# Kernel optimization log

Hardware: AMD Instinct MI355X
Metric: run time of the kernel (lower is better)

The kernel has to match this reference:

```python
import jax, jax.numpy as jnp
import numpy as np

MARGIN = 0.7
SINKHORN_ITERS = 500


def setup_inputs() -> dict:
    key = jax.random.key(0)
    k1, k2, k3, k4, k5 = jax.random.split(key, 5)
    D, m, n = 2048, 2048, 2048
    query_features = jax.random.normal(k1, (D, m), dtype=jnp.float32)
    target_features = jax.random.normal(k2, (D, n), dtype=jnp.float32)
    # positive marginals (mu.log() / nu.log() must be finite), normalized to sum 1
    qa = jax.random.uniform(k3, (m,), dtype=jnp.float32, minval=0.1, maxval=1.0)
    ta = jax.random.uniform(k4, (n,), dtype=jnp.float32, minval=0.1, maxval=1.0)
    query_attention = qa / qa.sum()
    target_attention = ta / ta.sum()
    # contrastive label: 1 = positive pair, 0 = negative
    label = (jax.random.uniform(k5, (m,)) < 0.5).astype(jnp.float32)
    return {
        "query_features": query_features,
        "query_attention": query_attention,
        "target_features": target_features,
        "target_attention": target_attention,
        "label": label,
    }


def _pairwise_sq_dist(x, y):
    # x: [m, D], y: [n, D] -> squared euclidean distances [m, n], clamped at 0
    x2 = jnp.sum(x * x, axis=1)[:, None]
    y2 = jnp.sum(y * y, axis=1)[None, :]
    d = x2 + y2 - 2.0 * (x @ y.T)
    return jnp.maximum(d, 0.0)


def _log_sinkhorn(Z, log_mu, log_nu, iters):
    # Z: [m, n]; log-space Sinkhorn, matching torch version with batch dim squeezed
    u0 = jnp.zeros_like(log_mu)
    v0 = jnp.zeros_like(log_nu)

    def body(_, uv):
        u, v = uv
        u = log_mu - jax.nn.logsumexp(Z + v[None, :], axis=1)
        v = log_nu - jax.nn.logsumexp(Z + u[:, None], axis=0)
        return (u, v)

    u, v = jax.lax.fori_loop(0, iters, body, (u0, v0))
    return Z + u[:, None] + v[None, :]


def reference(query_features, query_attention, target_features, target_attention, label):
    qf = query_features.T  # [m, D]
    tf = target_features.T  # [n, D]
    M = _pairwise_sq_dist(qf, tf)  # [m, n]
    logP = _log_sinkhorn(M, jnp.log(query_attention), jnp.log(target_attention), SINKHORN_ITERS)
    P = jnp.exp(logP)  # [m, n]
    # per-query-descriptor residual between weighted query and OT-transported target
    resid = query_attention[:, None] * qf - P @ tf  # [m, D]
    distance = jnp.linalg.norm(resid, axis=1)  # [m]
    loss = 0.5 * label * distance ** 2 + 0.5 * (1.0 - label) * jnp.maximum(MARGIN - distance, 0.0) ** 2
    return loss.sum()
```

## Files before the change

kernel.cpp:

```cpp
#include <hip/hip_runtime.h>
#include <math.h>

#define S 2048
#define MARGIN 0.7f
#define ITERS 500
#define NBLK 256
#define TPB 512
#define NREP 8

typedef unsigned long long u64;

#define SLOT_STRIDE 16384

__global__ __launch_bounds__(256) void init_marg_k(const float* __restrict__ qa,
                                                   const float* __restrict__ ta,
                                                   float* __restrict__ lmu,
                                                   float* __restrict__ lnu,
                                                   float* __restrict__ vt,
                                                   float* __restrict__ dist2,
                                                   u64* __restrict__ valU,
                                                   u64* __restrict__ valV) {
  int i = blockIdx.x * 256 + threadIdx.x;
  lmu[i] = __logf(qa[i]);
  lnu[i] = __logf(ta[i]);
  vt[i] = 0.f;
  dist2[i] = 0.f;
  const u64 poison = 0xFFFFFFFF00000000ull;
#pragma unroll
  for (int k = 0; k < 16; ++k) {
    valU[i + (k << 11)] = poison;
    valV[i + (k << 11)] = poison;
  }
}

__global__ __launch_bounds__(256) void colsumsq_k(const float* __restrict__ TF,
                                                  float* __restrict__ vt) {
  int jb = blockIdx.x & 7, dc = blockIdx.x >> 3;
  int j = jb * 256 + threadIdx.x;
  int d0 = dc * 256;
  float acc = 0.f;
  for (int d = d0; d < d0 + 256; ++d) {
    float v = TF[d * S + j];
    acc = fmaf(v, v, acc);
  }
  atomicAdd(&vt[j], acc);
}

__global__ __launch_bounds__(256) void pack_v0_k(const float* __restrict__ vt,
                                                 u64* __restrict__ valV) {
  int i = blockIdx.x * 256 + threadIdx.x;
  u64 w = (1ull << 32) | (u64)__float_as_uint(vt[i]);
#pragma unroll
  for (int r = 0; r < NREP; ++r) valV[(r << 11) + i] = w;
}

__global__ __launch_bounds__(256) void gemm_tn_k(const float* __restrict__ A,
                                                 const float* __restrict__ B,
                                                 float* __restrict__ C, float alpha) {
  __shared__ float As[16][128];
  __shared__ float Bs[16][128];
  int t = threadIdx.x;
  int i0 = blockIdx.y * 128, j0 = blockIdx.x * 128;
  int tx = t & 15, ty = t >> 4;
  float acc[8][8];
#pragma unroll
  for (int r = 0; r < 8; ++r)
#pragma unroll
    for (int c = 0; c < 8; ++c) acc[r][c] = 0.f;

  int e = t * 4;
  int dd0 = e >> 7, ii = e & 127;
  int dd1 = dd0 + 8;
  for (int k0 = 0; k0 < S; k0 += 16) {
    float4 a0 = *(const float4*)&A[(k0 + dd0) * S + i0 + ii];
    float4 b0 = *(const float4*)&B[(k0 + dd0) * S + j0 + ii];
    float4 a1 = *(const float4*)&A[(k0 + dd1) * S + i0 + ii];
    float4 b1 = *(const float4*)&B[(k0 + dd1) * S + j0 + ii];
    __syncthreads();
    *(float4*)&As[dd0][ii] = a0; *(float4*)&Bs[dd0][ii] = b0;
    *(float4*)&As[dd1][ii] = a1; *(float4*)&Bs[dd1][ii] = b1;
    __syncthreads();
#pragma unroll
    for (int kk = 0; kk < 16; ++kk) {
      float a[8], b[8];
      *(float4*)&a[0] = *(const float4*)&As[kk][ty * 8];
      *(float4*)&a[4] = *(const float4*)&As[kk][ty * 8 + 4];
      *(float4*)&b[0] = *(const float4*)&Bs[kk][tx * 4];
      *(float4*)&b[4] = *(const float4*)&Bs[kk][64 + tx * 4];
#pragma unroll
      for (int r = 0; r < 8; ++r)
#pragma unroll
        for (int c = 0; c < 8; ++c) acc[r][c] = fmaf(a[r], b[c], acc[r][c]);
    }
  }
#pragma unroll
  for (int r = 0; r < 8; ++r) {
    int i = i0 + ty * 8 + r;
    float4 o0 = make_float4(acc[r][0] * alpha, acc[r][1] * alpha, acc[r][2] * alpha, acc[r][3] * alpha);
    float4 o1 = make_float4(acc[r][4] * alpha, acc[r][5] * alpha, acc[r][6] * alpha, acc[r][7] * alpha);
    *(float4*)&C[i * S + j0 + tx * 4] = o0;
    *(float4*)&C[i * S + j0 + 64 + tx * 4] = o1;
  }
}

__global__ __launch_bounds__(256) void transpose_k(const float* __restrict__ in,
                                                   float* __restrict__ out) {
  __shared__ float tile[64][65];
  int i0 = blockIdx.y * 64, j0 = blockIdx.x * 64;
  int tx = threadIdx.x & 63, ty = threadIdx.x >> 6;
#pragma unroll
  for (int r = 0; r < 16; ++r) {
    int row = r * 4 + ty;
    tile[row][tx] = in[(i0 + row) * S + j0 + tx];
  }
  __syncthreads();
#pragma unroll
  for (int r = 0; r < 16; ++r) {
    int row = r * 4 + ty;
    out[(j0 + row) * S + i0 + tx] = tile[tx][row];
  }
}

#define PADD(P, A) P.x += A.x; P.y += A.y; P.z += A.z; P.w += A.w
#define PMAX(P) fmaxf(fmaxf(P.x, P.y), fmaxf(P.z, P.w))
#define PEXPS(P) (__expf(P.x - m) + __expf(P.y - m) + __expf(P.z - m) + __expf(P.w - m))
#define ALD(p) __hip_atomic_load((p), __ATOMIC_RELAXED, __HIP_MEMORY_SCOPE_AGENT)

__device__ __forceinline__ unsigned consume(const u64* __restrict__ base,
                                            unsigned ph,
                                            float* __restrict__ s_pot,
                                            unsigned* __restrict__ s_chgW,
                                            int t, int wv, int lane) {
  if (t < 64) {
    unsigned got = 0;
    const int L0 = t << 2;
    while (got != 0xFu) {
#pragma unroll
      for (int k = 0; k < 4; ++k)
        if (!(got & (1u << k)))
          if ((unsigned)(ALD(&base[(L0 + k) << 3]) >> 33) == ph)
            got |= 1u << k;
    }
  }
  __syncthreads();
  const int e = t << 2;
  u64 w0 = ALD(&base[e + 0]);
  u64 w1 = ALD(&base[e + 1]);
  u64 w2 = ALD(&base[e + 2]);
  u64 w3 = ALD(&base[e + 3]);
  unsigned ok = 0;
  do {
    if (!(ok & 1u)) { if ((unsigned)(w0 >> 33) == ph) ok |= 1u; else w0 = ALD(&base[e + 0]); }
    if (!(ok & 2u)) { if ((unsigned)(w1 >> 33) == ph) ok |= 2u; else w1 = ALD(&base[e + 1]); }
    if (!(ok & 4u)) { if ((unsigned)(w2 >> 33) == ph) ok |= 4u; else w2 = ALD(&base[e + 2]); }
    if (!(ok & 8u)) { if ((unsigned)(w3 >> 33) == ph) ok |= 8u; else w3 = ALD(&base[e + 3]); }
  } while (ok != 0xFu);
  unsigned chg = (unsigned)((w0 | w1 | w2 | w3) >> 32) & 1u;
  *(float4*)&s_pot[e] = make_float4(__uint_as_float((unsigned)w0),
                                    __uint_as_float((unsigned)w1),
                                    __uint_as_float((unsigned)w2),
                                    __uint_as_float((unsigned)w3));
  unsigned long long any = __ballot(chg != 0u);
  if (lane == 0) s_chgW[wv] = (any != 0ull) ? 1u : 0u;
  __syncthreads();
  return s_chgW[0] | s_chgW[1] | s_chgW[2] | s_chgW[3] |
         s_chgW[4] | s_chgW[5] | s_chgW[6] | s_chgW[7];
}

__device__ __forceinline__ float lse_row(const float* __restrict__ grow,
                                         const float* __restrict__ s_pot,
                                         int lane) {
  int j0 = lane << 2;
  float4 p0 = *(const float4*)&s_pot[j0];
  float4 p1 = *(const float4*)&s_pot[j0 + 256];
  float4 p2 = *(const float4*)&s_pot[j0 + 512];
  float4 p3 = *(const float4*)&s_pot[j0 + 768];
  float4 p4 = *(const float4*)&s_pot[j0 + 1024];
  float4 p5 = *(const float4*)&s_pot[j0 + 1280];
  float4 p6 = *(const float4*)&s_pot[j0 + 1536];
  float4 p7 = *(const float4*)&s_pot[j0 + 1792];
  float4 a0 = *(const float4*)&grow[j0];
  float4 a1 = *(const float4*)&grow[j0 + 256];
  float4 a2 = *(const float4*)&grow[j0 + 512];
  float4 a3 = *(const float4*)&grow[j0 + 768];
  float4 a4 = *(const float4*)&grow[j0 + 1024];
  float4 a5 = *(const float4*)&grow[j0 + 1280];
  float4 a6 = *(const float4*)&grow[j0 + 1536];
  float4 a7 = *(const float4*)&grow[j0 + 1792];
  PADD(p0, a0); PADD(p1, a1); PADD(p2, a2); PADD(p3, a3);
  PADD(p4, a4); PADD(p5, a5); PADD(p6, a6); PADD(p7, a7);
  float m0 = PMAX(p0), m1 = PMAX(p1), m2 = PMAX(p2), m3 = PMAX(p3);
  float m4 = PMAX(p4), m5 = PMAX(p5), m6 = PMAX(p6), m7 = PMAX(p7);
  m0 = fmaxf(m0, m1); m2 = fmaxf(m2, m3); m4 = fmaxf(m4, m5); m6 = fmaxf(m6, m7);
  float m = fmaxf(fmaxf(m0, m2), fmaxf(m4, m6));
#pragma unroll
  for (int off = 32; off; off >>= 1) m = fmaxf(m, __shfl_xor(m, off));
  float s = PEXPS(p0) + PEXPS(p1) + PEXPS(p2) + PEXPS(p3) +
            PEXPS(p4) + PEXPS(p5) + PEXPS(p6) + PEXPS(p7);
#pragma unroll
  for (int off = 32; off; off >>= 1) s += __shfl_xor(s, off);
  return m + __logf(s);
}

__global__ __launch_bounds__(TPB) void sinkhorn_k(
    const float* __restrict__ Gp, const float* __restrict__ GpT,
    const float* __restrict__ lmu, const float* __restrict__ lnu,
    float* __restrict__ ut, float* __restrict__ vt,
    u64* __restrict__ valU, u64* __restrict__ valV) {
  __shared__ float s_gu[8 * S];
  __shared__ float s_gv[8 * S];
  __shared__ float s_pot[S];
  __shared__ float s_res[8];
  __shared__ unsigned s_resC[8];
  __shared__ unsigned s_chgW[8];

  const int t = threadIdx.x;
  const int wv = t >> 6, lane = t & 63;
  const int bid = (int)blockIdx.x;
  const int row = (bid << 3) + wv;
  const int rep = bid & (NREP - 1);

  {
    const float* gu = Gp + (size_t)row * S;
    const float* gv = GpT + (size_t)row * S;
    float* lgu = s_gu + wv * S;
    float* lgv = s_gv + wv * S;
#pragma unroll
    for (int c = 0; c < 8; ++c) {
      int j = (lane << 2) + (c << 8);
      *(float4*)&lgu[j] = *(const float4*)&gu[j];
      *(float4*)&lgv[j] = *(const float4*)&gv[j];
    }
  }
  const float lmu_r = lmu[row];
  const float lnu_r = lnu[row];
  const float* grow_u = s_gu + wv * S;
  const float* grow_v = s_gv + wv * S;
  float prevU = __uint_as_float(0x7fc00000u);
  float prevV = prevU;
  float uLast = 0.f, vLast = 0.f;
  __syncthreads();

  for (int it = 0; it < ITERS; ++it) {
    const size_t so = (size_t)(it & 1) * SLOT_STRIDE;
    const unsigned phv = 2u * (unsigned)it;

    unsigned changed = consume(valV + so + ((size_t)rep << 11), phv,
                               s_pot, s_chgW, t, wv, lane);
    if (changed == 0u) break;
    {
      float nu = lmu_r - lse_row(grow_u, s_pot, lane);
      uLast = nu;
      if (lane == 0) {
        s_res[wv] = nu;
        s_resC[wv] = (__float_as_uint(nu) != __float_as_uint(prevU)) ? 1u : 0u;
        prevU = nu;
      }
    }
    __syncthreads();
    if (t < 64) {
      int jj = t & 7;
      u64 w = ((u64)(((phv + 1u) << 1) | s_resC[jj]) << 32) |
              (u64)__float_as_uint(s_res[jj]);
      __hip_atomic_store(&valU[so + ((size_t)(t >> 3) << 11) + (bid << 3) + jj],
                         w, __ATOMIC_RELAXED, __HIP_MEMORY_SCOPE_AGENT);
    }

    changed = consume(valU + so + ((size_t)rep << 11), phv + 1u,
                      s_pot, s_chgW, t, wv, lane);
    if (changed == 0u) break;
    {
      float nv = lnu_r - lse_row(grow_v, s_pot, lane);
      vLast = nv;
      if (lane == 0) {
        s_res[wv] = nv;
        s_resC[wv] = (__float_as_uint(nv) != __float_as_uint(prevV)) ? 1u : 0u;
        prevV = nv;
      }
    }
    __syncthreads();
    {
      const size_t so2 = (size_t)((it + 1) & 1) * SLOT_STRIDE;
      if (t < 64) {
        int jj = t & 7;
        u64 w = ((u64)(((phv + 2u) << 1) | s_resC[jj]) << 32) |
                (u64)__float_as_uint(s_res[jj]);
        __hip_atomic_store(&valV[so2 + ((size_t)(t >> 3) << 11) + (bid << 3) + jj],
                           w, __ATOMIC_RELAXED, __HIP_MEMORY_SCOPE_AGENT);
      }
    }
  }
  if (lane == 0) {
    ut[row] = uLast;
    vt[row] = vLast;
  }
}

__global__ __launch_bounds__(256) void rt_gemm_k(const float* __restrict__ TF,
                                                 const float* __restrict__ GpT,
                                                 const float* __restrict__ ut,
                                                 const float* __restrict__ vt,
                                                 float* __restrict__ RT) {
  __shared__ float As[16][128];
  __shared__ float Bs[16][128];
  int t = threadIdx.x;
  int d0 = blockIdx.y * 128, i0 = blockIdx.x * 128;
  int tx = t & 15, ty = t >> 4;
  float acc[8][8];
#pragma unroll
  for (int r = 0; r < 8; ++r)
#pragma unroll
    for (int c = 0; c < 8; ++c) acc[r][c] = 0.f;

  int akk = (t * 4) & 15, add0 = t >> 2;
  int eb = t * 4;
  int bkk0 = eb >> 7, bii = eb & 127, bkk1 = bkk0 + 8;
  float4 u4 = *(const float4*)&ut[i0 + bii];

  for (int k0 = 0; k0 < S; k0 += 16) {
    float4 av0 = *(const float4*)&TF[(d0 + add0) * S + k0 + akk];
    float4 av1 = *(const float4*)&TF[(d0 + add0 + 64) * S + k0 + akk];
    float4 g0 = *(const float4*)&GpT[(k0 + bkk0) * S + i0 + bii];
    float4 g1 = *(const float4*)&GpT[(k0 + bkk1) * S + i0 + bii];
    float v0 = vt[k0 + bkk0], v1 = vt[k0 + bkk1];
    __syncthreads();
    As[akk + 0][add0] = av0.x; As[akk + 1][add0] = av0.y;
    As[akk + 2][add0] = av0.z; As[akk + 3][add0] = av0.w;
    As[akk + 0][add0 + 64] = av1.x; As[akk + 1][add0 + 64] = av1.y;
    As[akk + 2][add0 + 64] = av1.z; As[akk + 3][add0 + 64] = av1.w;
    float4 p0 = make_float4(__expf(g0.x + u4.x + v0), __expf(g0.y + u4.y + v0),
                            __expf(g0.z + u4.z + v0), __expf(g0.w + u4.w + v0));
    float4 p1 = make_float4(__expf(g1.x + u4.x + v1), __expf(g1.y + u4.y + v1),
                            __expf(g1.z + u4.z + v1), __expf(g1.w + u4.w + v1));
    *(float4*)&Bs[bkk0][bii] = p0;
    *(float4*)&Bs[bkk1][bii] = p1;
    __syncthreads();
#pragma unroll
    for (int kk = 0; kk < 16; ++kk) {
      float a[8], b[8];
      *(float4*)&a[0] = *(const float4*)&As[kk][ty * 8];
      *(float4*)&a[4] = *(const float4*)&As[kk][ty * 8 + 4];
      *(float4*)&b[0] = *(const float4*)&Bs[kk][tx * 4];
      *(float4*)&b[4] = *(const float4*)&Bs[kk][64 + tx * 4];
#pragma unroll
      for (int r = 0; r < 8; ++r)
#pragma unroll
        for (int c = 0; c < 8; ++c) acc[r][c] = fmaf(a[r], b[c], acc[r][c]);
    }
  }
#pragma unroll
  for (int r = 0; r < 8; ++r) {
    int d = d0 + ty * 8 + r;
    *(float4*)&RT[d * S + i0 + tx * 4] = *(float4*)&acc[r][0];
    *(float4*)&RT[d * S + i0 + 64 + tx * 4] = *(float4*)&acc[r][4];
  }
}

__global__ __launch_bounds__(256) void dist2_partial_k(const float* __restrict__ QF,
                                                       const float* __restrict__ RT,
                                                       const float* __restrict__ qa,
                                                       float* __restrict__ dist2) {
  int ib = blockIdx.x & 7, dc = blockIdx.x >> 3;
  int i = ib * 256 + threadIdx.x;
  float qai = qa[i];
  float acc = 0.f;
  int d0 = dc * 256;
  for (int d = d0; d < d0 + 256; ++d) {
    float q = QF[d * S + i];
    float r = RT[d * S + i];
    float x = fmaf(qai, q, -r);
    acc = fmaf(x, x, acc);
  }
  atomicAdd(&dist2[i], acc);
}

__global__ __launch_bounds__(256) void loss_final_k(const float* __restrict__ dist2,
                                                    const float* __restrict__ label,
                                                    float* __restrict__ out) {
  int t = threadIdx.x;
  float acc = 0.f;
#pragma unroll
  for (int k = 0; k < 8; ++k) {
    int i = t + k * 256;
    float d2 = dist2[i];
    float dist = sqrtf(d2);
    float lab = label[i];
    float neg = fmaxf(MARGIN - dist, 0.f);
    acc += 0.5f * lab * d2 + 0.5f * (1.f - lab) * neg * neg;
  }
#pragma unroll
  for (int off = 32; off; off >>= 1) acc += __shfl_xor(acc, off);
  __shared__ float wsum[4];
  int wave = t >> 6, lane = t & 63;
  if (lane == 0) wsum[wave] = acc;
  __syncthreads();
  if (t == 0) out[0] = wsum[0] + wsum[1] + wsum[2] + wsum[3];
}

extern "C" void kernel_launch(void* const* d_in, const int* in_sizes, int n_in,
                              void* d_out, int out_size, void* d_ws, size_t ws_size,
                              hipStream_t stream) {
  const float* QF  = (const float*)d_in[0];
  const float* qa  = (const float*)d_in[1];
  const float* TF  = (const float*)d_in[2];
  const float* ta  = (const float*)d_in[3];
  const float* lab = (const float*)d_in[4];
  float* out = (float*)d_out;

  float* ws = (float*)d_ws;
  float* Gp    = ws;
  float* GpT   = Gp + S * S;
  float* ut    = GpT + S * S;
  float* vt    = ut + S;
  float* lmu   = vt + S;
  float* lnu   = lmu + S;
  float* dist2 = lnu + S;
  u64* valU = (u64*)(dist2 + S);
  u64* valV = valU + 2 * SLOT_STRIDE;

  init_marg_k<<<8, 256, 0, stream>>>(qa, ta, lmu, lnu, vt, dist2, valU, valV);
  colsumsq_k<<<64, 256, 0, stream>>>(TF, vt);
  pack_v0_k<<<8, 256, 0, stream>>>(vt, valV);
  gemm_tn_k<<<dim3(16, 16), 256, 0, stream>>>(QF, TF, Gp, -2.0f);
  transpose_k<<<dim3(32, 32), 256, 0, stream>>>(Gp, GpT);

  {
    const float* cGp = Gp; const float* cGpT = GpT;
    const float* clmu = lmu; const float* clnu = lnu;
    float* cut = ut; float* cvt = vt;
    u64* cvalU = valU; u64* cvalV = valV;
    void* kargs[] = {&cGp, &cGpT, &clmu, &clnu, &cut, &cvt, &cvalU, &cvalV};
    hipLaunchCooperativeKernel((const void*)sinkhorn_k, dim3(NBLK), dim3(TPB),
                               kargs, 0, stream);
  }

  rt_gemm_k<<<dim3(16, 16), 256, 0, stream>>>(TF, GpT, ut, vt, Gp);
  dist2_partial_k<<<64, 256, 0, stream>>>(QF, Gp, qa, dist2);
  loss_final_k<<<1, 256, 0, stream>>>(dist2, lab, out);
}
```

Before: 4.887 ms.

## Replace block barriers with per-wave ready flags and drop convergence early-exit

Removes the __syncthreads barriers in the persistent Sinkhorn kernel. Each wave now polls its own slice of the cross-block potential vector, writes it to a double-buffered shared array, and signals it through a workgroup-scope ready flag. Waves consume chunks as soon as they are ready and publish their results directly from lanes, with no staging through shared memory. The per-value 'changed' bit and the early break on convergence are dropped, so all 500 iterations always run, trading that possible shortcut for less intra-block synchronisation.

```diff
diff --git a/kernel.cpp b/kernel.cpp
--- a/kernel.cpp
+++ b/kernel.cpp
@@ -11,6 +11,9 @@
 typedef unsigned long long u64;
 
 #define SLOT_STRIDE 16384
+
+#define ALD(p) __hip_atomic_load((p), __ATOMIC_RELAXED, __HIP_MEMORY_SCOPE_AGENT)
+#define AST(p, v) __hip_atomic_store((p), (v), __ATOMIC_RELAXED, __HIP_MEMORY_SCOPE_AGENT)
 
 __global__ __launch_bounds__(256) void init_marg_k(const float* __restrict__ qa,
                                                    const float* __restrict__ ta,
@@ -49,7 +52,7 @@
 __global__ __launch_bounds__(256) void pack_v0_k(const float* __restrict__ vt,
                                                  u64* __restrict__ valV) {
   int i = blockIdx.x * 256 + threadIdx.x;
-  u64 w = (1ull << 32) | (u64)__float_as_uint(vt[i]);
+  u64 w = (u64)__float_as_uint(vt[i]);
 #pragma unroll
   for (int r = 0; r < NREP; ++r) valV[(r << 11) + i] = w;
 }
@@ -121,85 +124,64 @@
   }
 }
 
-#define PADD(P, A) P.x += A.x; P.y += A.y; P.z += A.z; P.w += A.w
 #define PMAX(P) fmaxf(fmaxf(P.x, P.y), fmaxf(P.z, P.w))
 #define PEXPS(P) (__expf(P.x - m) + __expf(P.y - m) + __expf(P.z - m) + __expf(P.w - m))
-#define ALD(p) __hip_atomic_load((p), __ATOMIC_RELAXED, __HIP_MEMORY_SCOPE_AGENT)
-
-__device__ __forceinline__ unsigned consume(const u64* __restrict__ base,
-                                            unsigned ph,
-                                            float* __restrict__ s_pot,
-                                            unsigned* __restrict__ s_chgW,
-                                            int t, int wv, int lane) {
-  if (t < 64) {
-    unsigned got = 0;
-    const int L0 = t << 2;
-    while (got != 0xFu) {
-#pragma unroll
-      for (int k = 0; k < 4; ++k)
-        if (!(got & (1u << k)))
-          if ((unsigned)(ALD(&base[(L0 + k) << 3]) >> 33) == ph)
-            got |= 1u << k;
-    }
-  }
-  __syncthreads();
-  const int e = t << 2;
+
+#define CHUNK(g, P)                                                            \
+  while (__hip_atomic_load(&s_ready[g], __ATOMIC_ACQUIRE,                      \
+                           __HIP_MEMORY_SCOPE_WORKGROUP) != ph) {}             \
+  {                                                                            \
+    float4 _q = *(const float4*)&s_pot[pb + ((g) << 8) + (lane << 2)];         \
+    float4 _a = *(const float4*)&grow[((g) << 8) + (lane << 2)];               \
+    P = make_float4(_q.x + _a.x, _q.y + _a.y, _q.z + _a.z, _q.w + _a.w);       \
+    mx = fmaxf(mx, PMAX(P));                                                   \
+  }
+
+__device__ __forceinline__ float pass_lse(const u64* __restrict__ base,
+                                          unsigned ph,
+                                          const float* __restrict__ grow,
+                                          float* __restrict__ s_pot,
+                                          unsigned* __restrict__ s_ready,
+                                          int wv, int lane, float lmarg) {
+  {
+    const int b = (wv << 5) + (lane & 31);
+    const int idx = (b << 3) + ((lane >> 5) << 2);
+    bool ok = false;
+    do {
+      if (!ok) ok = ((unsigned)(ALD(&base[idx]) >> 32) == ph);
+    } while (!__all(ok));
+  }
+  const int e = (wv << 8) + (lane << 2);
   u64 w0 = ALD(&base[e + 0]);
   u64 w1 = ALD(&base[e + 1]);
   u64 w2 = ALD(&base[e + 2]);
   u64 w3 = ALD(&base[e + 3]);
-  unsigned ok = 0;
+  unsigned ok4 = 0;
   do {
-    if (!(ok & 1u)) { if ((unsigned)(w0 >> 33) == ph) ok |= 1u; else w0 = ALD(&base[e + 0]); }
-    if (!(ok & 2u)) { if ((unsigned)(w1 >> 33) == ph) ok |= 2u; else w1 = ALD(&base[e + 1]); }
-    if (!(ok & 4u)) { if ((unsigned)(w2 >> 33) == ph) ok |= 4u; else w2 = ALD(&base[e + 2]); }
-    if (!(ok & 8u)) { if ((unsigned)(w3 >> 33) == ph) ok |= 8u; else w3 = ALD(&base[e + 3]); }
-  } while (ok != 0xFu);
-  unsigned chg = (unsigned)((w0 | w1 | w2 | w3) >> 32) & 1u;
-  *(float4*)&s_pot[e] = make_float4(__uint_as_float((unsigned)w0),
-                                    __uint_as_float((unsigned)w1),
-                                    __uint_as_float((unsigned)w2),
-                                    __uint_as_float((unsigned)w3));
-  unsigned long long any = __ballot(chg != 0u);
-  if (lane == 0) s_chgW[wv] = (any != 0ull) ? 1u : 0u;
-  __syncthreads();
-  return s_chgW[0] | s_chgW[1] | s_chgW[2] | s_chgW[3] |
-         s_chgW[4] | s_chgW[5] | s_chgW[6] | s_chgW[7];
-}
-
-__device__ __forceinline__ float lse_row(const float* __restrict__ grow,
-                                         const float* __restrict__ s_pot,
-                                         int lane) {
-  int j0 = lane << 2;
-  float4 p0 = *(const float4*)&s_pot[j0];
-  float4 p1 = *(const float4*)&s_pot[j0 + 256];
-  float4 p2 = *(const float4*)&s_pot[j0 + 512];
-  float4 p3 = *(const float4*)&s_pot[j0 + 768];
-  float4 p4 = *(const float4*)&s_pot[j0 + 1024];
-  float4 p5 = *(const float4*)&s_pot[j0 + 1280];
-  float4 p6 = *(const float4*)&s_pot[j0 + 1536];
-  float4 p7 = *(const float4*)&s_pot[j0 + 1792];
-  float4 a0 = *(const float4*)&grow[j0];
-  float4 a1 = *(const float4*)&grow[j0 + 256];
-  float4 a2 = *(const float4*)&grow[j0 + 512];
-  float4 a3 = *(const float4*)&grow[j0 + 768];
-  float4 a4 = *(const float4*)&grow[j0 + 1024];
-  float4 a5 = *(const float4*)&grow[j0 + 1280];
-  float4 a6 = *(const float4*)&grow[j0 + 1536];
-  float4 a7 = *(const float4*)&grow[j0 + 1792];
-  PADD(p0, a0); PADD(p1, a1); PADD(p2, a2); PADD(p3, a3);
-  PADD(p4, a4); PADD(p5, a5); PADD(p6, a6); PADD(p7, a7);
-  float m0 = PMAX(p0), m1 = PMAX(p1), m2 = PMAX(p2), m3 = PMAX(p3);
-  float m4 = PMAX(p4), m5 = PMAX(p5), m6 = PMAX(p6), m7 = PMAX(p7);
-  m0 = fmaxf(m0, m1); m2 = fmaxf(m2, m3); m4 = fmaxf(m4, m5); m6 = fmaxf(m6, m7);
-  float m = fmaxf(fmaxf(m0, m2), fmaxf(m4, m6));
-#pragma unroll
-  for (int off = 32; off; off >>= 1) m = fmaxf(m, __shfl_xor(m, off));
+    if (!(ok4 & 1u)) { if ((unsigned)(w0 >> 32) == ph) ok4 |= 1u; else w0 = ALD(&base[e + 0]); }
+    if (!(ok4 & 2u)) { if ((unsigned)(w1 >> 32) == ph) ok4 |= 2u; else w1 = ALD(&base[e + 1]); }
+    if (!(ok4 & 4u)) { if ((unsigned)(w2 >> 32) == ph) ok4 |= 4u; else w2 = ALD(&base[e + 2]); }
+    if (!(ok4 & 8u)) { if ((unsigned)(w3 >> 32) == ph) ok4 |= 8u; else w3 = ALD(&base[e + 3]); }
+  } while (ok4 != 0xFu);
+  const int pb = (int)(ph & 1u) << 11;
+  *(float4*)&s_pot[pb + e] = make_float4(__uint_as_float((unsigned)w0),
+                                         __uint_as_float((unsigned)w1),
+                                         __uint_as_float((unsigned)w2),
+                                         __uint_as_float((unsigned)w3));
+  __hip_atomic_store(&s_ready[wv], ph, __ATOMIC_RELEASE,
+                     __HIP_MEMORY_SCOPE_WORKGROUP);
+  float4 p0, p1, p2, p3, p4, p5, p6, p7;
+  float mx = -3.402823466e38f;
+  CHUNK(0, p0) CHUNK(1, p1) CHUNK(2, p2) CHUNK(3, p3)
+  CHUNK(4, p4) CHUNK(5, p5) CHUNK(6, p6) CHUNK(7, p7)
+#pragma unroll
+  for (int off = 32; off; off >>= 1) mx = fmaxf(mx, __shfl_xor(mx, off));
+  const float m = mx;
   float s = PEXPS(p0) + PEXPS(p1) + PEXPS(p2) + PEXPS(p3) +
             PEXPS(p4) + PEXPS(p5) + PEXPS(p6) + PEXPS(p7);
 #pragma unroll
   for (int off = 32; off; off >>= 1) s += __shfl_xor(s, off);
-  return m + __logf(s);
+  return lmarg - (m + __logf(s));
 }
 
 __global__ __launch_bounds__(TPB) void sinkhorn_k(
@@ -209,10 +191,8 @@
     u64* __restrict__ valU, u64* __restrict__ valV) {
   __shared__ float s_gu[8 * S];
   __shared__ float s_gv[8 * S];
-  __shared__ float s_pot[S];
-  __shared__ float s_res[8];
-  __shared__ unsigned s_resC[8];
-  __shared__ unsigned s_chgW[8];
+  __shared__ float s_pot[2 * S];
+  __shared__ unsigned s_ready[8];
 
   const int t = threadIdx.x;
   const int wv = t >> 6, lane = t & 63;
@@ -232,63 +212,33 @@
       *(float4*)&lgv[j] = *(const float4*)&gv[j];
     }
   }
+  if (t < 8) s_ready[t] = 0xFFFFFFFFu;
   const float lmu_r = lmu[row];
   const float lnu_r = lnu[row];
   const float* grow_u = s_gu + wv * S;
   const float* grow_v = s_gv + wv * S;
-  float prevU = __uint_as_float(0x7fc00000u);
-  float prevV = prevU;
   float uLast = 0.f, vLast = 0.f;
   __syncthreads();
 
   for (int it = 0; it < ITERS; ++it) {
     const size_t so = (size_t)(it & 1) * SLOT_STRIDE;
+    const size_t so2 = (size_t)((it + 1) & 1) * SLOT_STRIDE;
     const unsigned phv = 2u * (unsigned)it;
-
-    unsigned changed = consume(valV + so + ((size_t)rep << 11), phv,
-                               s_pot, s_chgW, t, wv, lane);
-    if (changed == 0u) break;
-    {
-      float nu = lmu_r - lse_row(grow_u, s_pot, lane);
-      uLast = nu;
-      if (lane == 0) {
-        s_res[wv] = nu;
-        s_resC[wv] = (__float_as_uint(nu) != __float_as_uint(prevU)) ? 1u : 0u;
-        prevU = nu;
-      }
-    }
-    __syncthreads();
-    if (t < 64) {
-      int jj = t & 7;
-      u64 w = ((u64)(((phv + 1u) << 1) | s_resC[jj]) << 32) |
-              (u64)__float_as_uint(s_res[jj]);
-      __hip_atomic_store(&valU[so + ((size_t)(t >> 3) << 11) + (bid << 3) + jj],
-                         w, __ATOMIC_RELAXED, __HIP_MEMORY_SCOPE_AGENT);
-    }
-
-    changed = consume(valU + so + ((size_t)rep << 11), phv + 1u,
-                      s_pot, s_chgW, t, wv, lane);
-    if (changed == 0u) break;
-    {
-      float nv = lnu_r - lse_row(grow_v, s_pot, lane);
-      vLast = nv;
-      if (lane == 0) {
-        s_res[wv] = nv;
-        s_resC[wv] = (__float_as_uint(nv) != __float_as_uint(prevV)) ? 1u : 0u;
-        prevV = nv;
-      }
-    }
-    __syncthreads();
-    {
-      const size_t so2 = (size_t)((it + 1) & 1) * SLOT_STRIDE;
-      if (t < 64) {
-        int jj = t & 7;
-        u64 w = ((u64)(((phv + 2u) << 1) | s_resC[jj]) << 32) |
-                (u64)__float_as_uint(s_res[jj]);
-        __hip_atomic_store(&valV[so2 + ((size_t)(t >> 3) << 11) + (bid << 3) + jj],
-                           w, __ATOMIC_RELAXED, __HIP_MEMORY_SCOPE_AGENT);
-      }
-    }
+    const unsigned phu = phv + 1u;
+
+    float nu = pass_lse(valV + so + ((size_t)rep << 11), phv, grow_u,
+                        s_pot, s_ready, wv, lane, lmu_r);
+    uLast = nu;
+    if (lane < 8)
+      AST(&valU[so + ((size_t)lane << 11) + row],
+          ((u64)phu << 32) | (u64)__float_as_uint(nu));
+
+    float nv = pass_lse(valU + so + ((size_t)rep << 11), phu, grow_v,
+                        s_pot, s_ready, wv, lane, lnu_r);
+    vLast = nv;
+    if (lane < 8)
+      AST(&valV[so2 + ((size_t)lane << 11) + row],
+          ((u64)(phv + 2u) << 32) | (u64)__float_as_uint(nv));
   }
   if (lane == 0) {
     ut[row] = uLast;
```

Measured after the change: 6.591 ms. 34.9% more time.
